# Kernel optimization log

Hardware: AMD Instinct MI355X
Metric: run time of the kernel (lower is better)

Reference implementation:

```python
import jax, jax.numpy as jnp
import numpy as np

EPS = 0.1
B, D, H = 1048576, 2, 64


def _lagrangian(xs, W0, b0, W1, b1, W2, b2, W3, b3):
    # xs: [2] single sample -> scalar Lagrangian L(q, v)
    h = jnp.tanh(xs @ W0 + b0)
    h = jnp.tanh(h @ W1 + b1)
    h = jnp.tanh(h @ W2 + b2)
    return (h @ W3 + b3)[0]


def setup_inputs() -> dict:
    key = jax.random.key(0)
    ks = jax.random.split(key, 9)
    def lin(k, fan_in, fan_out):
        # mimic nn.Linear default init U(-1/sqrt(fan_in), 1/sqrt(fan_in))
        bound = 1.0 / np.sqrt(fan_in)
        kw, kb = jax.random.split(k)
        W = jax.random.uniform(kw, (fan_in, fan_out), jnp.float32, -bound, bound)
        b = jax.random.uniform(kb, (fan_out,), jnp.float32, -bound, bound)
        return W, b
    W0, b0 = lin(ks[1], D, H)
    W1, b1 = lin(ks[2], H, H)
    W2, b2 = lin(ks[3], H, H)
    W3, b3 = lin(ks[4], H, 1)
    x = jax.random.normal(ks[0], (B, D), jnp.float32)
    return {"t": 0, "x": x, "W0": W0, "b0": b0, "W1": W1, "b1": b1,
            "W2": W2, "b2": b2, "W3": W3, "b3": b3}


def reference(t, x, W0, b0, W1, b1, W2, b2, W3, b3):
    lag = lambda xs: _lagrangian(xs, W0, b0, W1, b1, W2, b2, W3, b3)
    grad_all = jax.vmap(jax.grad(lag))(x)          # [B, 2]
    H_full = jax.vmap(jax.hessian(lag))(x)          # [B, 2, 2]
    dL_dq = grad_all[:, 0:1]                        # [B, 1]
    d2L_dqv = H_full[:, 1, 0:1]                     # d2L/(dv dq)
    d2L_dv2 = H_full[:, 1, 1:2]                     # d2L/dv2
    v = x[:, 1:2]
    a = (dL_dq - d2L_dqv * v) / (d2L_dv2 + EPS)
    return jnp.concatenate([v, a], axis=1)          # [B, 2]
```

## Files before the change

kernel.cpp:

```cpp
#include <hip/hip_runtime.h>
#include <hip/hip_fp16.h>

typedef _Float16 half8 __attribute__((ext_vector_type(8)));
typedef float    f32x4 __attribute__((ext_vector_type(4)));
typedef float    f32x2 __attribute__((ext_vector_type(2)));

#define EPSL 0.1f
#define LDSW 68
#define TWO_LOG2E 2.8853900817779268f

#if __has_builtin(__builtin_amdgcn_exp2f)
#define EXP2(x) __builtin_amdgcn_exp2f(x)
#else
#define EXP2(x) __expf((x) * 0.6931471805599453f)
#endif

__device__ __forceinline__ f32x2 tanh2s(f32x2 y) {
    f32x2 e;
    e.x = EXP2(y.x);
    e.y = EXP2(y.y);
    const f32x2 ep = e + 1.0f;
    f32x2 r;
    r.x = __builtin_amdgcn_rcpf(ep.x);
    r.y = __builtin_amdgcn_rcpf(ep.y);
    return 1.0f - 2.0f * r;
}

__device__ __forceinline__ unsigned int pk2(float a, float b) {
    union { __fp16 __attribute__((ext_vector_type(2))) h; unsigned int u; } v;
    v.h = __builtin_amdgcn_cvt_pkrtz(a, b);
    return v.u;
}
__device__ __forceinline__ f32x2 unpk2v(unsigned int u) {
    union { unsigned int u; __half2 h; } v; v.u = u;
    const float2 f = __half22float2(v.h);
    return (f32x2){f.x, f.y};
}
__device__ __forceinline__ f32x2 lo2(f32x4 v) { return __builtin_shufflevector(v, v, 0, 1); }
__device__ __forceinline__ f32x2 hi2(f32x4 v) { return __builtin_shufflevector(v, v, 2, 3); }

__global__ void pack_weights(const float* __restrict__ W1,
                             const float* __restrict__ W2,
                             _Float16* __restrict__ pk) {
    const int t = threadIdx.x;
    const int combo = blockIdx.x;
    const int nt  = combo & 3;
    const int kt  = (combo >> 2) & 1;
    const int mat = combo >> 3;
    const int q = t >> 4, r = t & 15;
    const int n = nt * 16 + r;
    const int m3 = (nt & 1) * 32 + (r >> 2) * 8 + ((nt >> 1) & 1) * 4 + (r & 3);
    _Float16 v[8];
    #pragma unroll
    for (int j = 0; j < 8; ++j) {
        const int k = kt * 32 + q * 8 + j;
        float x;
        if (mat == 0)      x = W1[k * 64 + n];
        else if (mat == 1) x = W2[k * 64 + n];
        else if (mat == 2) x = W2[n * 64 + k];
        else               x = W1[m3 * 64 + k];
        v[j] = (_Float16)x;
    }
    *(half8*)(pk + combo * 512 + t * 8) = *(const half8*)v;
}

extern "C" __global__ void __launch_bounds__(256)
__attribute__((amdgpu_waves_per_eu(4, 6)))
lnn_mfma(const float* __restrict__ x,
         const float* __restrict__ W0, const float* __restrict__ b0,
         const float* __restrict__ b1, const float* __restrict__ b2,
         const float* __restrict__ W3,
         const _Float16* __restrict__ pk,
         float* __restrict__ out)
{
    __shared__ unsigned int lds [64 * LDSW];

    const int t    = threadIdx.x & 63;
    const int w    = threadIdx.x >> 6;
    const int q    = t >> 4;
    const int r    = t & 15;
    const int wrow = w * 16;
    const long sbase = (long)blockIdx.x * 64 + wrow;

    const float2 xv = *(const float2*)(x + 2 * (sbase + r));
    const float x0 = xv.x, x1 = xv.y;

    auto ldpk = [&](int mat, int kt, int nt) -> half8 {
        return *(const half8*)(pk + ((mat * 2 + kt) * 4 + nt) * 512 + t * 8);
    };
    auto ldfrag = [&](int row, int kt, half8& vf, half8& tf) {
        const int off = row * LDSW + kt * 32 + q * 8;
        const uint4 A = *(const uint4*)&lds[off];
        const uint4 B = *(const uint4*)&lds[off + 4];
        union { unsigned int u[4]; half8 h; } cv, ct;
        cv.u[0] = __builtin_amdgcn_perm(A.y, A.x, 0x05040100u);
        cv.u[1] = __builtin_amdgcn_perm(A.w, A.z, 0x05040100u);
        cv.u[2] = __builtin_amdgcn_perm(B.y, B.x, 0x05040100u);
        cv.u[3] = __builtin_amdgcn_perm(B.w, B.z, 0x05040100u);
        ct.u[0] = __builtin_amdgcn_perm(A.y, A.x, 0x07060302u);
        ct.u[1] = __builtin_amdgcn_perm(A.w, A.z, 0x07060302u);
        ct.u[2] = __builtin_amdgcn_perm(B.y, B.x, 0x07060302u);
        ct.u[3] = __builtin_amdgcn_perm(B.w, B.z, 0x07060302u);
        vf = cv.h; tf = ct.h;
    };

    half8 ah0[2], at0[2];
    #pragma unroll
    for (int kt = 0; kt < 2; ++kt) {
        const int f = kt * 32 + q * 8;
        const float4 waA = *(const float4*)(W0 + f);
        const float4 waB = *(const float4*)(W0 + f + 4);
        const float4 wbA = *(const float4*)(W0 + 64 + f);
        const float4 wbB = *(const float4*)(W0 + 64 + f + 4);
        const float4 bbA = *(const float4*)(b0 + f);
        const float4 bbB = *(const float4*)(b0 + f + 4);
        const f32x2 wa2[4] = {{waA.x,waA.y},{waA.z,waA.w},{waB.x,waB.y},{waB.z,waB.w}};
        const f32x2 wb2[4] = {{wbA.x,wbA.y},{wbA.z,wbA.w},{wbB.x,wbB.y},{wbB.z,wbB.w}};
        const f32x2 bb2[4] = {{bbA.x,bbA.y},{bbA.z,bbA.w},{bbB.x,bbB.y},{bbB.z,bbB.w}};
        union { unsigned int u[4]; half8 h; } ph, pt;
        #pragma unroll
        for (int p = 0; p < 4; ++p) {
            const f32x2 z = x0 * wa2[p] + x1 * wb2[p] + bb2[p];
            const f32x2 h = tanh2s(z * TWO_LOG2E);
            const f32x2 A = 1.0f - h * h;
            const f32x2 tt = A * wb2[p];
            ph.u[p] = pk2(h.x, h.y);
            pt.u[p] = pk2(tt.x, tt.y);
        }
        ah0[kt] = ph.h; at0[kt] = pt.h;
    }

    f32x4 acc[4], tacc[4];
    #pragma unroll
    for (int nt = 0; nt < 4; ++nt) {
        const float bf = b1[nt * 16 + r];
        acc[nt]  = (f32x4){bf, bf, bf, bf};
        tacc[nt] = (f32x4){0, 0, 0, 0};
    }
    #pragma unroll
    for (int kt = 0; kt < 2; ++kt)
        #pragma unroll
        for (int nt = 0; nt < 4; ++nt) {
            const half8 bw = ldpk(0, kt, nt);
            acc[nt]  = __builtin_amdgcn_mfma_f32_16x16x32_f16(ah0[kt], bw, acc[nt], 0, 0, 0);
            tacc[nt] = __builtin_amdgcn_mfma_f32_16x16x32_f16(at0[kt], bw, tacc[nt], 0, 0, 0);
        }

    unsigned int h1p[4][4];
    #pragma unroll
    for (int nt = 0; nt < 4; ++nt) {
        const f32x2 zp[2] = {lo2(acc[nt]),  hi2(acc[nt])};
        const f32x2 tp[2] = {lo2(tacc[nt]), hi2(tacc[nt])};
        #pragma unroll
        for (int p = 0; p < 2; ++p) {
            const f32x2 h  = tanh2s(zp[p] * TWO_LOG2E);
            const f32x2 A  = 1.0f - h * h;
            const f32x2 th = A * tp[p];
            const unsigned int u0 = pk2(h.x, th.x);
            const unsigned int u1 = pk2(h.y, th.y);
            h1p[nt][2 * p]     = u0;
            h1p[nt][2 * p + 1] = u1;
            lds[(wrow + q * 4 + 2 * p)     * LDSW + nt * 16 + r] = u0;
            lds[(wrow + q * 4 + 2 * p + 1) * LDSW + nt * 16 + r] = u1;
        }
    }
    __builtin_amdgcn_wave_barrier();

    #pragma unroll
    for (int nt = 0; nt < 4; ++nt) {
        const float bf = b2[nt * 16 + r];
        acc[nt]  = (f32x4){bf, bf, bf, bf};
        tacc[nt] = (f32x4){0, 0, 0, 0};
    }
    #pragma unroll
    for (int kt = 0; kt < 2; ++kt) {
        half8 av, at;
        ldfrag(wrow + r, kt, av, at);
        #pragma unroll
        for (int nt = 0; nt < 4; ++nt) {
            const half8 bw = ldpk(1, kt, nt);
            acc[nt]  = __builtin_amdgcn_mfma_f32_16x16x32_f16(av, bw, acc[nt], 0, 0, 0);
            tacc[nt] = __builtin_amdgcn_mfma_f32_16x16x32_f16(at, bw, tacc[nt], 0, 0, 0);
        }
    }
    __builtin_amdgcn_wave_barrier();

    #pragma unroll
    for (int nt = 0; nt < 4; ++nt) {
        const float w3f = W3[nt * 16 + r];
        const f32x2 zp[2] = {lo2(acc[nt]),  hi2(acc[nt])};
        const f32x2 tp[2] = {lo2(tacc[nt]), hi2(tacc[nt])};
        #pragma unroll
        for (int p = 0; p < 2; ++p) {
            const f32x2 h  = tanh2s(zp[p] * TWO_LOG2E);
            const f32x2 A  = 1.0f - h * h;
            const f32x2 dz = A * w3f;
            const f32x2 t1 = h * tp[p];
            const f32x2 td = -2.0f * (dz * t1);
            lds[(wrow + q * 4 + 2 * p)     * LDSW + nt * 16 + r] = pk2(dz.x, td.x);
            lds[(wrow + q * 4 + 2 * p + 1) * LDSW + nt * 16 + r] = pk2(dz.y, td.y);
        }
    }
    __builtin_amdgcn_wave_barrier();

    #pragma unroll
    for (int nt = 0; nt < 4; ++nt) { acc[nt] = (f32x4){0,0,0,0}; tacc[nt] = (f32x4){0,0,0,0}; }
    #pragma unroll
    for (int kt = 0; kt < 2; ++kt) {
        half8 av, at;
        ldfrag(wrow + r, kt, av, at);
        #pragma unroll
        for (int nt = 0; nt < 4; ++nt) {
            const half8 bw = ldpk(2, kt, nt);
            acc[nt]  = __builtin_amdgcn_mfma_f32_16x16x32_f16(av, bw, acc[nt], 0, 0, 0);
            tacc[nt] = __builtin_amdgcn_mfma_f32_16x16x32_f16(at, bw, tacc[nt], 0, 0, 0);
        }
    }
    __builtin_amdgcn_wave_barrier();

    #pragma unroll
    for (int nt = 0; nt < 4; ++nt) {
        const f32x2 gp[2] = {lo2(acc[nt]),  hi2(acc[nt])};
        const f32x2 tp[2] = {lo2(tacc[nt]), hi2(tacc[nt])};
        #pragma unroll
        for (int p = 0; p < 2; ++p) {
            const unsigned int hu = __builtin_amdgcn_perm(h1p[nt][2*p+1], h1p[nt][2*p], 0x05040100u);
            const unsigned int tu = __builtin_amdgcn_perm(h1p[nt][2*p+1], h1p[nt][2*p], 0x07060302u);
            const f32x2 h  = unpk2v(hu);
            const f32x2 th = unpk2v(tu);
            const f32x2 A  = 1.0f - h * h;
            const f32x2 d1 = gp[p] * A;
            const f32x2 u2 = (gp[p] * h) * th;
            const f32x2 td = tp[p] * A + (-2.0f) * u2;
            lds[(wrow + q * 4 + 2 * p)     * LDSW + nt * 16 + r] = pk2(d1.x, td.x);
            lds[(wrow + q * 4 + 2 * p + 1) * LDSW + nt * 16 + r] = pk2(d1.y, td.y);
        }
    }
    __builtin_amdgcn_wave_barrier();

    #pragma unroll
    for (int mt = 0; mt < 4; ++mt) { acc[mt] = (f32x4){0,0,0,0}; tacc[mt] = (f32x4){0,0,0,0}; }
    #pragma unroll
    for (int kt = 0; kt < 2; ++kt) {
        half8 bd, btd;
        ldfrag(wrow + r, kt, bd, btd);
        #pragma unroll
        for (int mt = 0; mt < 4; ++mt) {
            const half8 aw = ldpk(3, kt, mt);
            acc[mt]  = __builtin_amdgcn_mfma_f32_16x16x32_f16(aw, bd,  acc[mt], 0, 0, 0);
            tacc[mt] = __builtin_amdgcn_mfma_f32_16x16x32_f16(aw, btd, tacc[mt], 0, 0, 0);
        }
    }

    f32x2 pg2 = {0, 0}, ph02 = {0, 0}, ph12 = {0, 0};
    #pragma unroll
    for (int mt = 0; mt < 4; ++mt) {
        const int kt = mt & 1;
        const int jb = ((mt >> 1) & 1) * 4;
        const int f  = kt * 32 + q * 8 + jb;
        const float4 waF = *(const float4*)(W0 + f);
        const float4 wbF = *(const float4*)(W0 + 64 + f);
        const f32x2 wa2[2] = {{waF.x, waF.y}, {waF.z, waF.w}};
        const f32x2 wb2[2] = {{wbF.x, wbF.y}, {wbF.z, wbF.w}};
        union { half8 h; unsigned int u[4]; } av; av.h = ah0[kt];
        const unsigned int hu[2] = {av.u[jb >> 1], av.u[(jb >> 1) + 1]};
        const f32x2 gp[2] = {lo2(acc[mt]),  hi2(acc[mt])};
        const f32x2 tp[2] = {lo2(tacc[mt]), hi2(tacc[mt])};
        #pragma unroll
        for (int p = 0; p < 2; ++p) {
            const f32x2 h   = unpk2v(hu[p]);
            const f32x2 A   = 1.0f - h * h;
            const f32x2 th0 = A * wb2[p];
            const f32x2 d0  = gp[p] * A;
            const f32x2 u2  = (gp[p] * h) * th0;
            const f32x2 td0 = tp[p] * A + (-2.0f) * u2;
            pg2  += wa2[p] * d0;
            ph02 += wa2[p] * td0;
            ph12 += wb2[p] * td0;
        }
    }
    float pg  = pg2.x  + pg2.y;
    float ph0 = ph02.x + ph02.y;
    float ph1 = ph12.x + ph12.y;
    pg  += __shfl_xor(pg, 16);  pg  += __shfl_xor(pg, 32);
    ph0 += __shfl_xor(ph0, 16); ph0 += __shfl_xor(ph0, 32);
    ph1 += __shfl_xor(ph1, 16); ph1 += __shfl_xor(ph1, 32);
    if (q == 0) {
        const float num = fmaf(-ph0, x1, pg);
        const float den = ph1 + EPSL;
        const float a = num * __builtin_amdgcn_rcpf(den);
        float2 o;
        o.x = x1;
        o.y = a;
        *(float2*)(out + 2 * (sbase + r)) = o;
    }
}

extern "C" void kernel_launch(void* const* d_in, const int* in_sizes, int n_in,
                              void* d_out, int out_size, void* d_ws, size_t ws_size,
                              hipStream_t stream) {
    const float* x  = (const float*)d_in[1];
    const float* W0 = (const float*)d_in[2];
    const float* b0 = (const float*)d_in[3];
    const float* W1 = (const float*)d_in[4];
    const float* b1 = (const float*)d_in[5];
    const float* W2 = (const float*)d_in[6];
    const float* b2 = (const float*)d_in[7];
    const float* W3 = (const float*)d_in[8];

    _Float16* pk = (_Float16*)d_ws;
    const int B = in_sizes[1] / 2;

    pack_weights<<<32, 64, 0, stream>>>(W1, W2, pk);
    lnn_mfma<<<B / 64, 256, 0, stream>>>(x, W0, b0, b1, b2, W3, pk, (float*)d_out);
}
```

Baseline: 226.7 us.

## Keep MLP activations in registers via transposed MFMA layout, drop LDS round-trips

Reformulates every layer as weight-times-activation (features as M, samples as N), with the packed weight fragments permuted so each MFMA output fragment maps directly onto the next layer's B-operand. The LDS staging buffer, its stores, fragment loads and perm shuffles between layers are removed. A dummy shared array that is never touched at runtime is added to cap occupancy, and the waves_per_eu attribute is dropped. The intent is to cut LDS traffic and instructions. The padding array may lower occupancy, and register pressure rises because activations now stay in registers.

After: 228.8 us. About the same (+0.9%).

```diff
diff --git a/kernel.cpp b/kernel.cpp
--- a/kernel.cpp
+++ b/kernel.cpp
@@ -6,7 +6,6 @@
 typedef float    f32x2 __attribute__((ext_vector_type(2)));
 
 #define EPSL 0.1f
-#define LDSW 68
 #define TWO_LOG2E 2.8853900817779268f
 
 #if __has_builtin(__builtin_amdgcn_exp2f)
@@ -39,33 +38,35 @@
 __device__ __forceinline__ f32x2 lo2(f32x4 v) { return __builtin_shufflevector(v, v, 0, 1); }
 __device__ __forceinline__ f32x2 hi2(f32x4 v) { return __builtin_shufflevector(v, v, 2, 3); }
 
+union frag_u { unsigned int u[4]; half8 h; };
+
 __global__ void pack_weights(const float* __restrict__ W1,
                              const float* __restrict__ W2,
                              _Float16* __restrict__ pk) {
     const int t = threadIdx.x;
     const int combo = blockIdx.x;
-    const int nt  = combo & 3;
+    const int mt  = combo & 3;
     const int kt  = (combo >> 2) & 1;
     const int mat = combo >> 3;
     const int q = t >> 4, r = t & 15;
-    const int n = nt * 16 + r;
-    const int m3 = (nt & 1) * 32 + (r >> 2) * 8 + ((nt >> 1) & 1) * 4 + (r & 3);
     _Float16 v[8];
     #pragma unroll
     for (int j = 0; j < 8; ++j) {
-        const int k = kt * 32 + q * 8 + j;
+        const int fk = (2 * kt + (j >> 2)) * 16 + 4 * q + (j & 3);
         float x;
-        if (mat == 0)      x = W1[k * 64 + n];
-        else if (mat == 1) x = W2[k * 64 + n];
-        else if (mat == 2) x = W2[n * 64 + k];
-        else               x = W1[m3 * 64 + k];
+        if (mat == 0)      x = W1[(kt * 32 + 8 * q + j) * 64 + mt * 16 + r];
+        else if (mat == 1) x = W2[fk * 64 + mt * 16 + r];
+        else if (mat == 2) x = W2[(mt * 16 + r) * 64 + fk];
+        else {
+            const int f0 = (mt & 1) * 32 + 8 * (r >> 2) + ((mt >> 1) & 1) * 4 + (r & 3);
+            x = W1[f0 * 64 + fk];
+        }
         v[j] = (_Float16)x;
     }
     *(half8*)(pk + combo * 512 + t * 8) = *(const half8*)v;
 }
 
 extern "C" __global__ void __launch_bounds__(256)
-__attribute__((amdgpu_waves_per_eu(4, 6)))
 lnn_mfma(const float* __restrict__ x,
          const float* __restrict__ W0, const float* __restrict__ b0,
          const float* __restrict__ b1, const float* __restrict__ b2,
@@ -73,35 +74,19 @@
          const _Float16* __restrict__ pk,
          float* __restrict__ out)
 {
-    __shared__ unsigned int lds [64 * LDSW];
-
-    const int t    = threadIdx.x & 63;
-    const int w    = threadIdx.x >> 6;
-    const int q    = t >> 4;
-    const int r    = t & 15;
-    const int wrow = w * 16;
-    const long sbase = (long)blockIdx.x * 64 + wrow;
+    __shared__ float occ_pad[7168];
+    if (blockIdx.x == 0xFFFFFFFFu) ((volatile float*)occ_pad)[threadIdx.x] = 1.0f;
+
+    const int t = threadIdx.x & 63;
+    const int q = t >> 4;
+    const int r = t & 15;
+    const long sbase = (long)blockIdx.x * 64 + (threadIdx.x >> 6) * 16;
 
     const float2 xv = *(const float2*)(x + 2 * (sbase + r));
     const float x0 = xv.x, x1 = xv.y;
 
-    auto ldpk = [&](int mat, int kt, int nt) -> half8 {
-        return *(const half8*)(pk + ((mat * 2 + kt) * 4 + nt) * 512 + t * 8);
-    };
-    auto ldfrag = [&](int row, int kt, half8& vf, half8& tf) {
-        const int off = row * LDSW + kt * 32 + q * 8;
-        const uint4 A = *(const uint4*)&lds[off];
-        const uint4 B = *(const uint4*)&lds[off + 4];
-        union { unsigned int u[4]; half8 h; } cv, ct;
-        cv.u[0] = __builtin_amdgcn_perm(A.y, A.x, 0x05040100u);
-        cv.u[1] = __builtin_amdgcn_perm(A.w, A.z, 0x05040100u);
-        cv.u[2] = __builtin_amdgcn_perm(B.y, B.x, 0x05040100u);
-        cv.u[3] = __builtin_amdgcn_perm(B.w, B.z, 0x05040100u);
-        ct.u[0] = __builtin_amdgcn_perm(A.y, A.x, 0x07060302u);
-        ct.u[1] = __builtin_amdgcn_perm(A.w, A.z, 0x07060302u);
-        ct.u[2] = __builtin_amdgcn_perm(B.y, B.x, 0x07060302u);
-        ct.u[3] = __builtin_amdgcn_perm(B.w, B.z, 0x07060302u);
-        vf = cv.h; tf = ct.h;
+    auto ldpk = [&](int mat, int kt, int mt) -> half8 {
+        return *(const half8*)(pk + ((mat * 2 + kt) * 4 + mt) * 512 + t * 8);
     };
 
     half8 ah0[2], at0[2];
@@ -132,125 +117,106 @@
 
     f32x4 acc[4], tacc[4];
     #pragma unroll
-    for (int nt = 0; nt < 4; ++nt) {
-        const float bf = b1[nt * 16 + r];
-        acc[nt]  = (f32x4){bf, bf, bf, bf};
-        tacc[nt] = (f32x4){0, 0, 0, 0};
-    }
-    #pragma unroll
-    for (int kt = 0; kt < 2; ++kt)
-        #pragma unroll
-        for (int nt = 0; nt < 4; ++nt) {
-            const half8 bw = ldpk(0, kt, nt);
-            acc[nt]  = __builtin_amdgcn_mfma_f32_16x16x32_f16(ah0[kt], bw, acc[nt], 0, 0, 0);
-            tacc[nt] = __builtin_amdgcn_mfma_f32_16x16x32_f16(at0[kt], bw, tacc[nt], 0, 0, 0);
-        }
-
-    unsigned int h1p[4][4];
-    #pragma unroll
-    for (int nt = 0; nt < 4; ++nt) {
-        const f32x2 zp[2] = {lo2(acc[nt]),  hi2(acc[nt])};
-        const f32x2 tp[2] = {lo2(tacc[nt]), hi2(tacc[nt])};
+    for (int mt = 0; mt < 4; ++mt) {
+        acc[mt]  = *(const f32x4*)(b1 + mt * 16 + 4 * q);
+        tacc[mt] = (f32x4){0, 0, 0, 0};
+    }
+    #pragma unroll
+    for (int kt = 0; kt < 2; ++kt)
+        #pragma unroll
+        for (int mt = 0; mt < 4; ++mt) {
+            const half8 aw = ldpk(0, kt, mt);
+            acc[mt]  = __builtin_amdgcn_mfma_f32_16x16x32_f16(aw, ah0[kt], acc[mt], 0, 0, 0);
+            tacc[mt] = __builtin_amdgcn_mfma_f32_16x16x32_f16(aw, at0[kt], tacc[mt], 0, 0, 0);
+        }
+
+    frag_u bh1[2], bt1[2];
+    #pragma unroll
+    for (int mt = 0; mt < 4; ++mt) {
+        const f32x2 zp[2] = {lo2(acc[mt]),  hi2(acc[mt])};
+        const f32x2 tp[2] = {lo2(tacc[mt]), hi2(tacc[mt])};
         #pragma unroll
         for (int p = 0; p < 2; ++p) {
             const f32x2 h  = tanh2s(zp[p] * TWO_LOG2E);
             const f32x2 A  = 1.0f - h * h;
             const f32x2 th = A * tp[p];
-            const unsigned int u0 = pk2(h.x, th.x);
-            const unsigned int u1 = pk2(h.y, th.y);
-            h1p[nt][2 * p]     = u0;
-            h1p[nt][2 * p + 1] = u1;
-            lds[(wrow + q * 4 + 2 * p)     * LDSW + nt * 16 + r] = u0;
-            lds[(wrow + q * 4 + 2 * p + 1) * LDSW + nt * 16 + r] = u1;
-        }
-    }
-    __builtin_amdgcn_wave_barrier();
-
-    #pragma unroll
-    for (int nt = 0; nt < 4; ++nt) {
-        const float bf = b2[nt * 16 + r];
-        acc[nt]  = (f32x4){bf, bf, bf, bf};
-        tacc[nt] = (f32x4){0, 0, 0, 0};
-    }
-    #pragma unroll
-    for (int kt = 0; kt < 2; ++kt) {
-        half8 av, at;
-        ldfrag(wrow + r, kt, av, at);
-        #pragma unroll
-        for (int nt = 0; nt < 4; ++nt) {
-            const half8 bw = ldpk(1, kt, nt);
-            acc[nt]  = __builtin_amdgcn_mfma_f32_16x16x32_f16(av, bw, acc[nt], 0, 0, 0);
-            tacc[nt] = __builtin_amdgcn_mfma_f32_16x16x32_f16(at, bw, tacc[nt], 0, 0, 0);
-        }
-    }
-    __builtin_amdgcn_wave_barrier();
-
-    #pragma unroll
-    for (int nt = 0; nt < 4; ++nt) {
-        const float w3f = W3[nt * 16 + r];
-        const f32x2 zp[2] = {lo2(acc[nt]),  hi2(acc[nt])};
-        const f32x2 tp[2] = {lo2(tacc[nt]), hi2(tacc[nt])};
+            bh1[mt >> 1].u[2 * (mt & 1) + p] = pk2(h.x, h.y);
+            bt1[mt >> 1].u[2 * (mt & 1) + p] = pk2(th.x, th.y);
+        }
+    }
+
+    #pragma unroll
+    for (int mt = 0; mt < 4; ++mt) {
+        acc[mt]  = *(const f32x4*)(b2 + mt * 16 + 4 * q);
+        tacc[mt] = (f32x4){0, 0, 0, 0};
+    }
+    #pragma unroll
+    for (int kt = 0; kt < 2; ++kt)
+        #pragma unroll
+        for (int mt = 0; mt < 4; ++mt) {
+            const half8 aw = ldpk(1, kt, mt);
+            acc[mt]  = __builtin_amdgcn_mfma_f32_16x16x32_f16(aw, bh1[kt].h, acc[mt], 0, 0, 0);
+            tacc[mt] = __builtin_amdgcn_mfma_f32_16x16x32_f16(aw, bt1[kt].h, tacc[mt], 0, 0, 0);
+        }
+
+    frag_u bh2[2], bt2[2];
+    #pragma unroll
+    for (int mt = 0; mt < 4; ++mt) {
+        const float4 w3v = *(const float4*)(W3 + mt * 16 + 4 * q);
+        const f32x2 w3p[2] = {{w3v.x, w3v.y}, {w3v.z, w3v.w}};
+        const f32x2 zp[2] = {lo2(acc[mt]),  hi2(acc[mt])};
+        const f32x2 tp[2] = {lo2(tacc[mt]), hi2(tacc[mt])};
         #pragma unroll
         for (int p = 0; p < 2; ++p) {
             const f32x2 h  = tanh2s(zp[p] * TWO_LOG2E);
             const f32x2 A  = 1.0f - h * h;
-            const f32x2 dz = A * w3f;
+            const f32x2 dz = A * w3p[p];
             const f32x2 t1 = h * tp[p];
             const f32x2 td = -2.0f * (dz * t1);
-            lds[(wrow + q * 4 + 2 * p)     * LDSW + nt * 16 + r] = pk2(dz.x, td.x);
-            lds[(wrow + q * 4 + 2 * p + 1) * LDSW + nt * 16 + r] = pk2(dz.y, td.y);
-        }
-    }
-    __builtin_amdgcn_wave_barrier();
-
-    #pragma unroll
-    for (int nt = 0; nt < 4; ++nt) { acc[nt] = (f32x4){0,0,0,0}; tacc[nt] = (f32x4){0,0,0,0}; }
-    #pragma unroll
-    for (int kt = 0; kt < 2; ++kt) {
-        half8 av, at;
-        ldfrag(wrow + r, kt, av, at);
-        #pragma unroll
-        for (int nt = 0; nt < 4; ++nt) {
-            const half8 bw = ldpk(2, kt, nt);
-            acc[nt]  = __builtin_amdgcn_mfma_f32_16x16x32_f16(av, bw, acc[nt], 0, 0, 0);
-            tacc[nt] = __builtin_amdgcn_mfma_f32_16x16x32_f16(at, bw, tacc[nt], 0, 0, 0);
-        }
-    }
-    __builtin_amdgcn_wave_barrier();
-
-    #pragma unroll
-    for (int nt = 0; nt < 4; ++nt) {
-        const f32x2 gp[2] = {lo2(acc[nt]),  hi2(acc[nt])};
-        const f32x2 tp[2] = {lo2(tacc[nt]), hi2(tacc[nt])};
-        #pragma unroll
-        for (int p = 0; p < 2; ++p) {
-            const unsigned int hu = __builtin_amdgcn_perm(h1p[nt][2*p+1], h1p[nt][2*p], 0x05040100u);
-            const unsigned int tu = __builtin_amdgcn_perm(h1p[nt][2*p+1], h1p[nt][2*p], 0x07060302u);
-            const f32x2 h  = unpk2v(hu);
-            const f32x2 th = unpk2v(tu);
+            bh2[mt >> 1].u[2 * (mt & 1) + p] = pk2(dz.x, dz.y);
+            bt2[mt >> 1].u[2 * (mt & 1) + p] = pk2(td.x, td.y);
+        }
+    }
+
+    #pragma unroll
+    for (int mt = 0; mt < 4; ++mt) { acc[mt] = (f32x4){0,0,0,0}; tacc[mt] = (f32x4){0,0,0,0}; }
+    #pragma unroll
+    for (int kt = 0; kt < 2; ++kt)
+        #pragma unroll
+        for (int mt = 0; mt < 4; ++mt) {
+            const half8 aw = ldpk(2, kt, mt);
+            acc[mt]  = __builtin_amdgcn_mfma_f32_16x16x32_f16(aw, bh2[kt].h, acc[mt], 0, 0, 0);
+            tacc[mt] = __builtin_amdgcn_mfma_f32_16x16x32_f16(aw, bt2[kt].h, tacc[mt], 0, 0, 0);
+        }
+
+    frag_u bd[2], btd[2];
+    #pragma unroll
+    for (int mt = 0; mt < 4; ++mt) {
+        const f32x2 gp[2] = {lo2(acc[mt]),  hi2(acc[mt])};
+        const f32x2 tp[2] = {lo2(tacc[mt]), hi2(tacc[mt])};
+        #pragma unroll
+        for (int p = 0; p < 2; ++p) {
+            const f32x2 h  = unpk2v(bh1[mt >> 1].u[2 * (mt & 1) + p]);
+            const f32x2 th = unpk2v(bt1[mt >> 1].u[2 * (mt & 1) + p]);
             const f32x2 A  = 1.0f - h * h;
             const f32x2 d1 = gp[p] * A;
             const f32x2 u2 = (gp[p] * h) * th;
             const f32x2 td = tp[p] * A + (-2.0f) * u2;
-            lds[(wrow + q * 4 + 2 * p)     * LDSW + nt * 16 + r] = pk2(d1.x, td.x);
-            lds[(wrow + q * 4 + 2 * p + 1) * LDSW + nt * 16 + r] = pk2(d1.y, td.y);
-        }
-    }
-    __builtin_amdgcn_wave_barrier();
+            bd[mt >> 1].u[2 * (mt & 1) + p]  = pk2(d1.x, d1.y);
+            btd[mt >> 1].u[2 * (mt & 1) + p] = pk2(td.x, td.y);
+        }
+    }
 
     #pragma unroll
     for (int mt = 0; mt < 4; ++mt) { acc[mt] = (f32x4){0,0,0,0}; tacc[mt] = (f32x4){0,0,0,0}; }
     #pragma unroll
-    for (int kt = 0; kt < 2; ++kt) {
-        half8 bd, btd;
-        ldfrag(wrow + r, kt, bd, btd);
+    for (int kt = 0; kt < 2; ++kt)
         #pragma unroll
         for (int mt = 0; mt < 4; ++mt) {
             const half8 aw = ldpk(3, kt, mt);
-            acc[mt]  = __builtin_amdgcn_mfma_f32_16x16x32_f16(aw, bd,  acc[mt], 0, 0, 0);
-            tacc[mt] = __builtin_amdgcn_mfma_f32_16x16x32_f16(aw, btd, tacc[mt], 0, 0, 0);
-        }
-    }
+            acc[mt]  = __builtin_amdgcn_mfma_f32_16x16x32_f16(aw, bd[kt].h,  acc[mt], 0, 0, 0);
+            tacc[mt] = __builtin_amdgcn_mfma_f32_16x16x32_f16(aw, btd[kt].h, tacc[mt], 0, 0, 0);
+        }
 
     f32x2 pg2 = {0, 0}, ph02 = {0, 0}, ph12 = {0, 0};
     #pragma unroll
```
